# Kernel tuning notes

Measured on AMD Instinct MI355X. Metric: run time of the kernel, lower is better.

The kernel has to match this reference:

```python
import jax, jax.numpy as jnp
import numpy as np
import math

NUM_HEADS = 16

def _alibi_slopes(num_heads):
    def pow2_slopes(n):
        start = 2.0 ** (-(2.0 ** (-(math.log2(n) - 3))))
        return [start * (start ** i) for i in range(n)]
    if math.log2(num_heads).is_integer():
        slopes = pow2_slopes(num_heads)
    else:
        cp2 = 2 ** int(math.floor(math.log2(num_heads)))
        slopes = pow2_slopes(cp2)
        extra = [slopes[0] * 2.0 ** (-(i - 1) / (num_heads - cp2))
                 for i in range(1, num_heads - cp2 + 1)]
        slopes = slopes + extra
    return jnp.asarray(np.array(slopes, dtype=np.float32))  # [H]

def setup_inputs() -> dict:
    key = jax.random.key(0)
    attention_scores = jax.random.normal(key, (2, NUM_HEADS, 2048, 2048), dtype=jnp.float32)
    return {"attention_scores": attention_scores}

def reference(attention_scores):
    B, H, S, _ = attention_scores.shape
    slopes = _alibi_slopes(H)  # [H]
    pos = jnp.arange(S)
    # relative_positions = -(|j - i|), shape [S, S]
    rel = -jnp.abs(pos[None, :] - pos[:, None]).astype(attention_scores.dtype)
    bias = slopes[:, None, None] * rel[None, :, :]  # [H, S, S]
    return attention_scores + bias[None, :, :, :]
```

## Files before the change

### kernel.cpp

```cpp
#include <hip/hip_runtime.h>


#define S_LOG2 11
#define ROW4_LOG2 9
#define H_MASK 15

__global__ __launch_bounds__(256) void alibi_bias_kernel(
    const float* __restrict__ in, float* __restrict__ out, long long n4) {
    long long idx    = (long long)blockIdx.x * blockDim.x + threadIdx.x;
    long long stride = (long long)gridDim.x * blockDim.x;
    const float4* __restrict__ in4  = reinterpret_cast<const float4*>(in);
    float4* __restrict__       out4 = reinterpret_cast<float4*>(out);

    for (long long f = idx; f < n4; f += stride) {
        int  jv  = (int)(f & ((1 << ROW4_LOG2) - 1));
        long long row = f >> ROW4_LOG2;
        int  i   = (int)(row & ((1 << S_LOG2) - 1));
        int  h   = (int)((row >> S_LOG2) & H_MASK);

        float slope = exp2f(-0.5f * (float)(h + 1));

        float4 v = in4[f];
        int j0 = jv << 2;
        v.x -= slope * fabsf((float)(j0 + 0 - i));
        v.y -= slope * fabsf((float)(j0 + 1 - i));
        v.z -= slope * fabsf((float)(j0 + 2 - i));
        v.w -= slope * fabsf((float)(j0 + 3 - i));
        out4[f] = v;
    }
}

extern "C" void kernel_launch(void* const* d_in, const int* in_sizes, int n_in,
                              void* d_out, int out_size, void* d_ws, size_t ws_size,
                              hipStream_t stream) {
    const float* in = (const float*)d_in[0];
    float* out = (float*)d_out;

    long long n  = (long long)out_size;
    long long n4 = n >> 2;

    const int block = 256;
    long long want = (n4 + block - 1) / block;
    int grid = (int)(want < 2048 ? want : 2048);

    alibi_bias_kernel<<<grid, block, 0, stream>>>(in, out, n4);
}
```

Measured before the change: 223.4 us.

## Assign fixed 16-row tiles per block with unrolled nontemporal vector loads/stores

Replaces the grid-stride loop with one block per 16 rows, so the head slope and row index are computed once per block. Each thread issues four independent 16-byte nontemporal loads before its stores, to raise memory-level parallelism and bypass cache pollution. The launch now assumes the element count is an exact multiple of the tile size, with the shape hardcoded.

```diff
diff --git a/kernel.cpp b/kernel.cpp
--- a/kernel.cpp
+++ b/kernel.cpp
@@ -1,32 +1,68 @@
 #include <hip/hip_runtime.h>
 
 
-#define S_LOG2 11
-#define ROW4_LOG2 9
-#define H_MASK 15
+typedef float f32x4 __attribute__((ext_vector_type(4)));
 
 __global__ __launch_bounds__(256) void alibi_bias_kernel(
-    const float* __restrict__ in, float* __restrict__ out, long long n4) {
-    long long idx    = (long long)blockIdx.x * blockDim.x + threadIdx.x;
-    long long stride = (long long)gridDim.x * blockDim.x;
-    const float4* __restrict__ in4  = reinterpret_cast<const float4*>(in);
-    float4* __restrict__       out4 = reinterpret_cast<float4*>(out);
+    const float* __restrict__ in, float* __restrict__ out) {
+    const int i_base = (blockIdx.x << 4) & 2047;
+    const int h      = (blockIdx.x >> 7) & 15;
+    const float slope = exp2f(-0.5f * (float)(h + 1));
 
-    for (long long f = idx; f < n4; f += stride) {
-        int  jv  = (int)(f & ((1 << ROW4_LOG2) - 1));
-        long long row = f >> ROW4_LOG2;
-        int  i   = (int)(row & ((1 << S_LOG2) - 1));
-        int  h   = (int)((row >> S_LOG2) & H_MASK);
+    const long long base4 = (long long)blockIdx.x << 13;
+    const f32x4* __restrict__ in4  = reinterpret_cast<const f32x4*>(in)  + base4;
+    f32x4* __restrict__       out4 = reinterpret_cast<f32x4*>(out) + base4;
 
-        float slope = exp2f(-0.5f * (float)(h + 1));
+    const int tid = threadIdx.x;
 
-        float4 v = in4[f];
-        int j0 = jv << 2;
-        v.x -= slope * fabsf((float)(j0 + 0 - i));
-        v.y -= slope * fabsf((float)(j0 + 1 - i));
-        v.z -= slope * fabsf((float)(j0 + 2 - i));
-        v.w -= slope * fabsf((float)(j0 + 3 - i));
-        out4[f] = v;
+    for (int it = 0; it < 8; ++it) {
+        int l0 = (it << 10) + tid;
+        int l1 = l0 + 256;
+        int l2 = l0 + 512;
+        int l3 = l0 + 768;
+
+        f32x4 v0 = __builtin_nontemporal_load(&in4[l0]);
+        f32x4 v1 = __builtin_nontemporal_load(&in4[l1]);
+        f32x4 v2 = __builtin_nontemporal_load(&in4[l2]);
+        f32x4 v3 = __builtin_nontemporal_load(&in4[l3]);
+
+        {
+            int i = i_base + (l0 >> 9);
+            float d = (float)((l0 & 511) * 4 - i);
+            v0.x -= slope * fabsf(d);
+            v0.y -= slope * fabsf(d + 1.0f);
+            v0.z -= slope * fabsf(d + 2.0f);
+            v0.w -= slope * fabsf(d + 3.0f);
+        }
+        {
+            int i = i_base + (l1 >> 9);
+            float d = (float)((l1 & 511) * 4 - i);
+            v1.x -= slope * fabsf(d);
+            v1.y -= slope * fabsf(d + 1.0f);
+            v1.z -= slope * fabsf(d + 2.0f);
+            v1.w -= slope * fabsf(d + 3.0f);
+        }
+        {
+            int i = i_base + (l2 >> 9);
+            float d = (float)((l2 & 511) * 4 - i);
+            v2.x -= slope * fabsf(d);
+            v2.y -= slope * fabsf(d + 1.0f);
+            v2.z -= slope * fabsf(d + 2.0f);
+            v2.w -= slope * fabsf(d + 3.0f);
+        }
+        {
+            int i = i_base + (l3 >> 9);
+            float d = (float)((l3 & 511) * 4 - i);
+            v3.x -= slope * fabsf(d);
+            v3.y -= slope * fabsf(d + 1.0f);
+            v3.z -= slope * fabsf(d + 2.0f);
+            v3.w -= slope * fabsf(d + 3.0f);
+        }
+
+        __builtin_nontemporal_store(v0, &out4[l0]);
+        __builtin_nontemporal_store(v1, &out4[l1]);
+        __builtin_nontemporal_store(v2, &out4[l2]);
+        __builtin_nontemporal_store(v3, &out4[l3]);
     }
 }
 
@@ -36,12 +72,8 @@
     const float* in = (const float*)d_in[0];
     float* out = (float*)d_out;
 
-    long long n  = (long long)out_size;
-    long long n4 = n >> 2;
+    long long n4 = (long long)out_size >> 2;
+    int grid = (int)(n4 >> 13);
 
-    const int block = 256;
-    long long want = (n4 + block - 1) / block;
-    int grid = (int)(want < 2048 ? want : 2048);
-
-    alibi_bias_kernel<<<grid, block, 0, stream>>>(in, out, n4);
+    alibi_bias_kernel<<<grid, 256, 0, stream>>>(in, out);
 }
```

Result: faster. 202.3 us (-9.4%).

## Tile 16 rows per block with nontemporal prefetching loads and stores

Applied to the files above, without the earlier changes.

Replaces the grid-stride loop with a fixed mapping where each block owns 16 consecutive rows of one head and derives the row and head from the block index. Loads are double-buffered one iteration ahead, and all loads and stores use nontemporal hints to stream past the cache. The bias is computed incrementally with FMA from a running float offset instead of per-element index decoding. The grid size now assumes the input is an exact multiple of 8192 float4s with S=2048 and H=16, with no bounds checks.

```diff
diff --git a/kernel.cpp b/kernel.cpp
--- a/kernel.cpp
+++ b/kernel.cpp
@@ -1,32 +1,58 @@
 #include <hip/hip_runtime.h>
 
 
-#define S_LOG2 11
-#define ROW4_LOG2 9
-#define H_MASK 15
+typedef float f32x4 __attribute__((ext_vector_type(4)));
+
+__device__ __forceinline__ void apply4(f32x4& v, float d, float ns) {
+    v.x = fmaf(ns, fabsf(d),        v.x);
+    v.y = fmaf(ns, fabsf(d + 1.0f), v.y);
+    v.z = fmaf(ns, fabsf(d + 2.0f), v.z);
+    v.w = fmaf(ns, fabsf(d + 3.0f), v.w);
+}
 
 __global__ __launch_bounds__(256) void alibi_bias_kernel(
-    const float* __restrict__ in, float* __restrict__ out, long long n4) {
-    long long idx    = (long long)blockIdx.x * blockDim.x + threadIdx.x;
-    long long stride = (long long)gridDim.x * blockDim.x;
-    const float4* __restrict__ in4  = reinterpret_cast<const float4*>(in);
-    float4* __restrict__       out4 = reinterpret_cast<float4*>(out);
+    const float* __restrict__ in, float* __restrict__ out) {
+    const int i_base = (blockIdx.x << 4) & 2047;
+    const int h      = (blockIdx.x >> 7) & 15;
+    const float nslope = -exp2f(-0.5f * (float)(h + 1));
 
-    for (long long f = idx; f < n4; f += stride) {
-        int  jv  = (int)(f & ((1 << ROW4_LOG2) - 1));
-        long long row = f >> ROW4_LOG2;
-        int  i   = (int)(row & ((1 << S_LOG2) - 1));
-        int  h   = (int)((row >> S_LOG2) & H_MASK);
+    const long long base4 = (long long)blockIdx.x << 13;
+    const f32x4* __restrict__ in4  = reinterpret_cast<const f32x4*>(in)  + base4;
+    f32x4* __restrict__       out4 = reinterpret_cast<f32x4*>(out) + base4;
 
-        float slope = exp2f(-0.5f * (float)(h + 1));
+    const int tid = threadIdx.x;
 
-        float4 v = in4[f];
-        int j0 = jv << 2;
-        v.x -= slope * fabsf((float)(j0 + 0 - i));
-        v.y -= slope * fabsf((float)(j0 + 1 - i));
-        v.z -= slope * fabsf((float)(j0 + 2 - i));
-        v.w -= slope * fabsf((float)(j0 + 3 - i));
-        out4[f] = v;
+    f32x4 a0 = __builtin_nontemporal_load(&in4[tid]);
+    f32x4 a1 = __builtin_nontemporal_load(&in4[tid + 256]);
+    f32x4 a2 = __builtin_nontemporal_load(&in4[tid + 512]);
+    f32x4 a3 = __builtin_nontemporal_load(&in4[tid + 768]);
+
+    float d = (float)((tid << 2) - i_base);
+
+#pragma unroll
+    for (int it = 0; it < 8; ++it) {
+        f32x4 b0, b1, b2, b3;
+        if (it < 7) {
+            int l = ((it + 1) << 10) + tid;
+            b0 = __builtin_nontemporal_load(&in4[l]);
+            b1 = __builtin_nontemporal_load(&in4[l + 256]);
+            b2 = __builtin_nontemporal_load(&in4[l + 512]);
+            b3 = __builtin_nontemporal_load(&in4[l + 768]);
+        }
+
+        apply4(a0, d,           nslope);
+        apply4(a1, d + 1024.0f, nslope);
+        apply4(a2, d - 1.0f,    nslope);
+        apply4(a3, d + 1023.0f, nslope);
+
+        int s = (it << 10) + tid;
+        __builtin_nontemporal_store(a0, &out4[s]);
+        __builtin_nontemporal_store(a1, &out4[s + 256]);
+        __builtin_nontemporal_store(a2, &out4[s + 512]);
+        __builtin_nontemporal_store(a3, &out4[s + 768]);
+
+        a0 = b0; a1 = b1; a2 = b2; a3 = b3;
+        d -= 2.0f;
     }
 }
 
@@ -36,12 +62,8 @@
     const float* in = (const float*)d_in[0];
     float* out = (float*)d_out;
 
-    long long n  = (long long)out_size;
-    long long n4 = n >> 2;
+    long long n4 = (long long)out_size >> 2;
+    int grid = (int)(n4 >> 13);
 
-    const int block = 256;
-    long long want = (n4 + block - 1) / block;
-    int grid = (int)(want < 2048 ? want : 2048);
-
-    alibi_bias_kernel<<<grid, block, 0, stream>>>(in, out, n4);
+    alibi_bias_kernel<<<grid, 256, 0, stream>>>(in, out);
 }
```

New measurement: 189.9 us. 15.0% less time.
